# Optimization experiments

Measured on AMD Instinct MI355X. Metric: run time of the kernel, lower is better.

## Reference

```python
import jax, jax.numpy as jnp
import numpy as np

EMBED_DIM = 1024
N_HEADS = 16


def setup_inputs() -> dict:
    key = jax.random.key(0)
    k1, k2, k3 = jax.random.split(key, 3)
    B, T, C = 4, 2048, EMBED_DIM
    x0 = jax.random.normal(k1, (B, T, C), dtype=jnp.float32)
    # Linear weights stored as (in, out) so y = x @ W, matching torch Linear math.
    w_attn = jax.random.normal(k2, (C, 3 * C), dtype=jnp.float32) * (1.0 / np.sqrt(C))
    w_proj = jax.random.normal(k3, (C, C), dtype=jnp.float32) * (1.0 / np.sqrt(C))
    return {"x0": x0, "w_attn": w_attn, "w_proj": w_proj}


def reference(x0, w_attn, w_proj):
    B, T, C = x0.shape
    H = N_HEADS
    D = C // H  # head dim
    qkv = x0 @ w_attn                      # [B, T, 3C]
    q, k, v = jnp.split(qkv, 3, axis=-1)
    # [B, T, C] -> [B, H, T, D]
    q = q.reshape(B, T, H, D).transpose(0, 2, 1, 3)
    k = k.reshape(B, T, H, D).transpose(0, 2, 1, 3)
    v = v.reshape(B, T, H, D).transpose(0, 2, 1, 3)
    scale = 1.0 / np.sqrt(D)
    attn = jnp.einsum('bhqd,bhkd->bhqk', q, k) * scale  # [B, H, T, T]
    causal = jnp.tril(jnp.ones((T, T), dtype=bool))
    attn = jnp.where(causal[None, None, :, :], attn, -jnp.inf)
    attn = jax.nn.softmax(attn, axis=-1)
    y = jnp.einsum('bhqk,bhkd->bhqd', attn, v)           # [B, H, T, D]
    y = y.transpose(0, 2, 1, 3).reshape(B, T, C)
    return y @ w_proj
```

## Files before the change

### kernel.cpp

```cpp
#include <hip/hip_runtime.h>

#define TSEQ 2048
#define NB 4
#define NH 16
#define HD 64
#define CEMB 1024
#define MROWS (NB*TSEQ)

typedef _Float16 half8 __attribute__((ext_vector_type(8)));
typedef _Float16 half4_t __attribute__((ext_vector_type(4)));
typedef float floatx4 __attribute__((ext_vector_type(4)));

__device__ __forceinline__ floatx4 mfma16x32(half8 a, half8 b, floatx4 c) {
    return __builtin_amdgcn_mfma_f32_16x16x32_f16(a, b, c, 0, 0, 0);
}

__device__ __forceinline__ void async16(const _Float16* g, _Float16* l) {
    __builtin_amdgcn_global_load_lds((const __attribute__((address_space(1))) void*)g,
                                     (__attribute__((address_space(3))) void*)l, 16, 0, 0);
}

__global__ __launch_bounds__(256) void cvt_fp32_fp16(const float* __restrict__ in,
                                                     _Float16* __restrict__ out) {
    size_t i = ((size_t)blockIdx.x * 256 + threadIdx.x) * 8;
    float4 a = *(const float4*)(in + i);
    float4 b = *(const float4*)(in + i + 4);
    half8 h;
    h[0] = (_Float16)a.x; h[1] = (_Float16)a.y; h[2] = (_Float16)a.z; h[3] = (_Float16)a.w;
    h[4] = (_Float16)b.x; h[5] = (_Float16)b.y; h[6] = (_Float16)b.z; h[7] = (_Float16)b.w;
    *(half8*)(out + i) = h;
}

__global__ __launch_bounds__(256) void transpose_cvt(const float* __restrict__ in,
                                                     _Float16* __restrict__ out,
                                                     int R, int Ccols) {
    __shared__ float tile[32][33];
    int bx = blockIdx.x;
    int by = blockIdx.y;
    int tx = threadIdx.x, ty = threadIdx.y;
    int x = bx * 32 + tx;
#pragma unroll
    for (int i = 0; i < 32; i += 8) {
        int y = by * 32 + ty + i;
        tile[ty + i][tx] = in[(size_t)y * Ccols + x];
    }
    __syncthreads();
#pragma unroll
    for (int i = 0; i < 32; i += 8) {
        int oc = bx * 32 + ty + i;
        int orow = by * 32 + tx;
        out[(size_t)oc * R + orow] = (_Float16)tile[tx][ty + i];
    }
}

template<int MODE, int BM>
__global__ __launch_bounds__(BM * 2, 4) void gemm_nt(const _Float16* __restrict__ A,
                                                     const _Float16* __restrict__ Bt,
                                                     float* __restrict__ Cf,
                                                     _Float16* __restrict__ Ch,
                                                     _Float16* __restrict__ VTh,
                                                     int N, int K) {
    __shared__ __align__(16) _Float16 As[2][BM * 32];
    __shared__ __align__(16) _Float16 Bs[2][4096];

    const int tid = threadIdx.x;
    const int wv = tid >> 6, lane = tid & 63;
    const int wm = (BM == 256) ? (wv & 3) : (wv >> 1);
    const int wn = (BM == 256) ? (wv >> 2) : (wv & 1);
    const int l16 = lane & 15, lq = lane >> 4;

    const int pid = blockIdx.x + gridDim.x * blockIdx.y;
    const int nn = gridDim.y;
    const int pig = 8 * nn;
    const int gid = pid / pig;
    const int rem = pid - gid * pig;
    const int bm = gid * 8 + (rem & 7);
    const int bn = rem >> 3;

    const int srow = lane >> 2;
    const int scol = ((lane & 3) ^ ((lane >> 3) & 3)) * 8;
    const _Float16* Abase = A + (size_t)(bm * BM) * K;
    const _Float16* Bbase = Bt + (size_t)(bn * 128) * K;

    const floatx4 zero = {0.f, 0.f, 0.f, 0.f};
    floatx4 acc[4][4];
#pragma unroll
    for (int i = 0; i < 4; i++)
#pragma unroll
        for (int j = 0; j < 4; j++) acc[i][j] = zero;

    auto stage = [&](int bf, int k0) {
#pragma unroll
        for (int cc = 0; cc < 2; cc++) {
            const int c = wv * 2 + cc;
            const size_t gofs = (size_t)(c * 16 + srow) * K + k0 + scol;
            async16(Abase + gofs, &As[bf][c * 512]);
        }
        if (BM == 256) {
            const int c = wv;
            const size_t gofs = (size_t)(c * 16 + srow) * K + k0 + scol;
            async16(Bbase + gofs, &Bs[bf][c * 512]);
        } else {
#pragma unroll
            for (int cc = 0; cc < 2; cc++) {
                const int c = wv * 2 + cc;
                const size_t gofs = (size_t)(c * 16 + srow) * K + k0 + scol;
                async16(Bbase + gofs, &Bs[bf][c * 512]);
            }
        }
    };

    stage(0, 0);
    int buf = 0;
    const int sw = (lq ^ ((l16 >> 1) & 3)) * 8;
    for (int k0 = 0; k0 < K; k0 += 32) {
        __syncthreads();
        if (k0 + 32 < K) stage(buf ^ 1, k0 + 32);
        half8 af[4], bf[4];
#pragma unroll
        for (int i = 0; i < 4; i++) {
            af[i] = *(const half8*)&As[buf][(wm * 64 + i * 16 + l16) * 32 + sw];
            bf[i] = *(const half8*)&Bs[buf][(wn * 64 + i * 16 + l16) * 32 + sw];
        }
#pragma unroll
        for (int i = 0; i < 4; i++)
#pragma unroll
            for (int j = 0; j < 4; j++)
                acc[i][j] = mfma16x32(af[i], bf[j], acc[i][j]);
        buf ^= 1;
    }

    if (MODE == 1) {
#pragma unroll
        for (int i = 0; i < 4; i++) {
            int row = bm * BM + wm * 64 + i * 16 + lq * 4;
#pragma unroll
            for (int j = 0; j < 4; j++) {
                int col = bn * 128 + wn * 64 + j * 16 + l16;
#pragma unroll
                for (int r = 0; r < 4; r++)
                    Cf[(size_t)(row + r) * N + col] = acc[i][j][r];
            }
        }
    } else {
        const int which = bn >> 3;
        if (which < 2) {
#pragma unroll
            for (int j = 0; j < 4; j++) {
                int n = bn * 128 + wn * 64 + j * 16 + l16;
                int c = n & 1023, h = c >> 6, d = c & 63;
                _Float16* dst = Ch + (size_t)which * ((size_t)MROWS * CEMB)
                                   + (size_t)h * (TSEQ * HD) + d;
#pragma unroll
                for (int i = 0; i < 4; i++) {
                    int row = bm * BM + wm * 64 + i * 16 + lq * 4;
#pragma unroll
                    for (int r = 0; r < 4; r++) {
                        int m = row + r;
                        int b = m >> 11, t = m & 2047;
                        dst[(size_t)b * (NH * TSEQ * HD) + (size_t)t * HD] = (_Float16)acc[i][j][r];
                    }
                }
            }
        } else {
#pragma unroll
            for (int j = 0; j < 4; j++) {
                int n = bn * 128 + wn * 64 + j * 16 + l16;
                int c = n & 1023, h = c >> 6, d = c & 63;
#pragma unroll
                for (int i = 0; i < 4; i++) {
                    int m0 = bm * BM + wm * 64 + i * 16 + lq * 4;
                    int b = m0 >> 11, t = m0 & 2047;
                    half4_t pk;
#pragma unroll
                    for (int r = 0; r < 4; r++) pk[r] = (_Float16)acc[i][j][r];
                    *(half4_t*)&VTh[(((size_t)(b * NH + h)) * HD + d) * TSEQ + t] = pk;
                }
            }
        }
    }
}

__global__ __launch_bounds__(512, 4) void attn_fwd(const _Float16* __restrict__ Qg,
                                                   const _Float16* __restrict__ Kg,
                                                   const _Float16* __restrict__ VTg,
                                                   _Float16* __restrict__ Y) {
    __shared__ __align__(16) _Float16 Ks[2][4096];
    __shared__ __align__(16) _Float16 Vt[2][4096];

    const int tid = threadIdx.x;
    const int w = tid >> 6, lane = tid & 63;
    const int l16 = lane & 15, quad = lane >> 4;
    const int bh = blockIdx.y;
    const int x = blockIdx.x;
    const int b = bh >> 4, h = bh & 15;
    const int qt = (b < 2) ? x : (7 - x);

    const _Float16* Qb = Qg + (size_t)bh * TSEQ * HD;
    const _Float16* Kb = Kg + (size_t)bh * TSEQ * HD;
    const _Float16* Vb = VTg + (size_t)bh * HD * TSEQ;

    const _Float16 ksc = (_Float16)(0.125f * 1.44269504089f);
    const floatx4 zero = {0.f, 0.f, 0.f, 0.f};

    half8 qf[2][2];
#pragma unroll
    for (int g = 0; g < 2; g++) {
        const _Float16* qrow = Qb + (size_t)(qt * 256 + g * 128 + w * 16 + l16) * HD;
        qf[g][0] = *(const half8*)(qrow + quad * 8);
        qf[g][1] = *(const half8*)(qrow + 32 + quad * 8);
#pragma unroll
        for (int e = 0; e < 8; e++) { qf[g][0][e] *= ksc; qf[g][1][e] *= ksc; }
    }

    floatx4 o[2][4];
#pragma unroll
    for (int g = 0; g < 2; g++)
#pragma unroll
        for (int dt = 0; dt < 4; dt++) o[g][dt] = zero;
    float lsum[2] = {0.f, 0.f};

    const int srow8 = lane >> 3;
    const int scol8 = ((lane & 7) ^ (lane >> 3)) * 8;

    auto stage = [&](int bf, int kt2) {
        const int row = w * 8 + srow8;
        async16(Kb + (size_t)(kt2 * 64 + row) * HD + scol8, &Ks[bf][w * 512]);
        async16(Vb + (size_t)row * TSEQ + kt2 * 64 + scol8, &Vt[bf][w * 512]);
    };

    const int kmax = 4 * qt + 3;
    stage(0, 0);
    int buf = 0;
    for (int kt = 0; kt <= kmax; ++kt) {
        __syncthreads();
        if (kt < kmax) stage(buf ^ 1, kt + 1);

        half8 kf0[4], kf1[4];
#pragma unroll
        for (int nj = 0; nj < 4; nj++) {
            const int rb = (nj * 16 + l16) * 64;
            kf0[nj] = *(const half8*)&Ks[buf][rb + ((quad ^ (l16 & 7)) * 8)];
            kf1[nj] = *(const half8*)&Ks[buf][rb + (((quad ^ 4) ^ (l16 & 7)) * 8)];
        }

        const bool doA = (kt <= 4 * qt + 1);
        half8 pf[2][2];
#pragma unroll
        for (int g = 0; g < 2; g++) {
            if (g == 0 && !doA) continue;
            floatx4 st[4];
#pragma unroll
            for (int nj = 0; nj < 4; nj++) {
                floatx4 t = mfma16x32(kf0[nj], qf[g][0], zero);
                st[nj] = mfma16x32(kf1[nj], qf[g][1], t);
            }
            if (kt * 64 + 63 > qt * 256 + g * 128 + w * 16) {
                const int klim = qt * 256 + g * 128 + w * 16 + l16 - kt * 64;
#pragma unroll
                for (int nj = 0; nj < 4; nj++)
#pragma unroll
                    for (int r = 0; r < 4; r++) {
                        int key = nj * 16 + quad * 4 + r;
                        if (key > klim) st[nj][r] = -1e30f;
                    }
            }
#pragma unroll
            for (int nj = 0; nj < 4; nj++)
#pragma unroll
                for (int r = 0; r < 4; r++) {
                    float p = __builtin_amdgcn_exp2f(st[nj][r]);
                    lsum[g] += p;
                    pf[g][nj >> 1][(nj & 1) * 4 + r] = (_Float16)p;
                }
        }

#pragma unroll
        for (int u = 0; u < 2; u++) {
#pragma unroll
            for (int dt = 0; dt < 4; dt++) {
                const int rb = (dt * 16 + l16) * 64;
                const int g0 = u * 4 + (quad >> 1);
                const int sub = (quad & 1) * 4;
                half4_t lo = *(const half4_t*)&Vt[buf][rb + ((g0 ^ (l16 & 7)) * 8 + sub)];
                half4_t hi = *(const half4_t*)&Vt[buf][rb + (((g0 + 2) ^ (l16 & 7)) * 8 + sub)];
                half8 vf;
                vf[0] = lo[0]; vf[1] = lo[1]; vf[2] = lo[2]; vf[3] = lo[3];
                vf[4] = hi[0]; vf[5] = hi[1]; vf[6] = hi[2]; vf[7] = hi[3];
                if (doA) o[0][dt] = mfma16x32(pf[0][u], vf, o[0][dt]);
                o[1][dt] = mfma16x32(pf[1][u], vf, o[1][dt]);
            }
        }
        buf ^= 1;
    }

#pragma unroll
    for (int g = 0; g < 2; g++) {
        float lt = lsum[g];
        lt += __shfl_xor(lt, 16);
        lt += __shfl_xor(lt, 32);
        float linv[4];
#pragma unroll
        for (int r = 0; r < 4; r++) linv[r] = 1.0f / __shfl(lt, quad * 4 + r);
#pragma unroll
        for (int dt = 0; dt < 4; dt++)
#pragma unroll
            for (int r = 0; r < 4; r++) {
                int q = qt * 256 + g * 128 + w * 16 + quad * 4 + r;
                int d = dt * 16 + l16;
                Y[((size_t)(b * TSEQ + q)) * CEMB + h * HD + d] = (_Float16)(o[g][dt][r] * linv[r]);
            }
    }
}

extern "C" void kernel_launch(void* const* d_in, const int* in_sizes, int n_in,
                              void* d_out, int out_size, void* d_ws, size_t ws_size,
                              hipStream_t stream) {
    const float* x0     = (const float*)d_in[0];
    const float* w_attn = (const float*)d_in[1];
    const float* w_proj = (const float*)d_in[2];
    float* out = (float*)d_out;

    _Float16* xh  = (_Float16*)d_ws;
    _Float16* wqt = xh  + (size_t)MROWS * CEMB;
    _Float16* wpt = wqt + (size_t)3 * CEMB * CEMB;
    _Float16* qh  = wpt + (size_t)CEMB * CEMB;
    _Float16* kh  = qh  + (size_t)MROWS * CEMB;
    _Float16* vt  = kh  + (size_t)MROWS * CEMB;
    _Float16* yh  = vt  + (size_t)MROWS * CEMB;

    cvt_fp32_fp16<<<(MROWS * CEMB) / (256 * 8), 256, 0, stream>>>(x0, xh);
    transpose_cvt<<<dim3(3 * CEMB / 32, CEMB / 32), dim3(32, 8), 0, stream>>>(w_attn, wqt, CEMB, 3 * CEMB);
    transpose_cvt<<<dim3(CEMB / 32, CEMB / 32), dim3(32, 8), 0, stream>>>(w_proj, wpt, CEMB, CEMB);

    gemm_nt<0, 256><<<dim3(MROWS / 256, 3 * CEMB / 128), 512, 0, stream>>>(xh, wqt, nullptr, qh, vt, 3 * CEMB, CEMB);
    attn_fwd<<<dim3(TSEQ / 256, NB * NH), 512, 0, stream>>>(qh, kh, vt, yh);
    gemm_nt<1, 128><<<dim3(MROWS / 128, CEMB / 128), 256, 0, stream>>>(yh, wpt, out, nullptr, nullptr, CEMB, CEMB);
}
```

Measured before the change: 252.5 us.

## Rewrite GEMM as 4-stage async pipeline with 128x256 tiles

Replaces the double-buffered GEMM with a four-slot LDS ring that prefetches three k-steps ahead, using explicit vmcnt waits, raw barriers, scheduling barriers and raised priority around the MFMA block. Both the QKV and output projections now use 128x256 output tiles with 512 threads, each warp holding a 64x64 sub-tile. The aim is to hide global-load latency behind matrix math and cut the number of block-wide syncs. In exchange it uses more LDS per block, which lowers occupancy, and the output projection gets fewer, larger blocks.

```diff
diff --git a/kernel.cpp b/kernel.cpp
--- a/kernel.cpp
+++ b/kernel.cpp
@@ -53,21 +53,20 @@
     }
 }
 
-template<int MODE, int BM>
-__global__ __launch_bounds__(BM * 2, 4) void gemm_nt(const _Float16* __restrict__ A,
-                                                     const _Float16* __restrict__ Bt,
-                                                     float* __restrict__ Cf,
-                                                     _Float16* __restrict__ Ch,
-                                                     _Float16* __restrict__ VTh,
-                                                     int N, int K) {
-    __shared__ __align__(16) _Float16 As[2][BM * 32];
-    __shared__ __align__(16) _Float16 Bs[2][4096];
+template<int MODE>
+__global__ __launch_bounds__(512, 2) void gemm_nt8(const _Float16* __restrict__ A,
+                                                   const _Float16* __restrict__ Bt,
+                                                   float* __restrict__ Cf,
+                                                   _Float16* __restrict__ Ch,
+                                                   _Float16* __restrict__ VTh,
+                                                   int N, int K) {
+    __shared__ __align__(16) _Float16 As[4][128 * 32];
+    __shared__ __align__(16) _Float16 Bs[4][256 * 32];
 
     const int tid = threadIdx.x;
     const int wv = tid >> 6, lane = tid & 63;
-    const int wm = (BM == 256) ? (wv & 3) : (wv >> 1);
-    const int wn = (BM == 256) ? (wv >> 2) : (wv & 1);
-    const int l16 = lane & 15, lq = lane >> 4;
+    const int wm = wv >> 2, wn = wv & 3;
+    const int l16 = lane & 15, quad = lane >> 4;
 
     const int pid = blockIdx.x + gridDim.x * blockIdx.y;
     const int nn = gridDim.y;
@@ -77,10 +76,17 @@
     const int bm = gid * 8 + (rem & 7);
     const int bn = rem >> 3;
 
-    const int srow = lane >> 2;
-    const int scol = ((lane & 3) ^ ((lane >> 3) & 3)) * 8;
-    const _Float16* Abase = A + (size_t)(bm * BM) * K;
-    const _Float16* Bbase = Bt + (size_t)(bn * 128) * K;
+    const int rA = tid >> 2;
+    const int kA = ((tid & 3) ^ ((rA >> 1) & 3)) * 8;
+    const _Float16* Ag  = A  + (size_t)(bm * 128 + rA) * K + kA;
+    const _Float16* Bg0 = Bt + (size_t)(bn * 256 + rA) * K + kA;
+    const _Float16* Bg1 = Bg0 + (size_t)128 * K;
+
+    auto stage = [&](int slot, int ss) {
+        async16(Ag  + ss * 32, &As[slot][wv * 512]);
+        async16(Bg0 + ss * 32, &Bs[slot][wv * 512]);
+        async16(Bg1 + ss * 32, &Bs[slot][4096 + wv * 512]);
+    };
 
     const floatx4 zero = {0.f, 0.f, 0.f, 0.f};
     floatx4 acc[4][4];
@@ -89,71 +95,62 @@
 #pragma unroll
         for (int j = 0; j < 4; j++) acc[i][j] = zero;
 
-    auto stage = [&](int bf, int k0) {
-#pragma unroll
-        for (int cc = 0; cc < 2; cc++) {
-            const int c = wv * 2 + cc;
-            const size_t gofs = (size_t)(c * 16 + srow) * K + k0 + scol;
-            async16(Abase + gofs, &As[bf][c * 512]);
-        }
-        if (BM == 256) {
-            const int c = wv;
-            const size_t gofs = (size_t)(c * 16 + srow) * K + k0 + scol;
-            async16(Bbase + gofs, &Bs[bf][c * 512]);
-        } else {
-#pragma unroll
-            for (int cc = 0; cc < 2; cc++) {
-                const int c = wv * 2 + cc;
-                const size_t gofs = (size_t)(c * 16 + srow) * K + k0 + scol;
-                async16(Bbase + gofs, &Bs[bf][c * 512]);
-            }
-        }
-    };
-
-    stage(0, 0);
-    int buf = 0;
-    const int sw = (lq ^ ((l16 >> 1) & 3)) * 8;
-    for (int k0 = 0; k0 < K; k0 += 32) {
-        __syncthreads();
-        if (k0 + 32 < K) stage(buf ^ 1, k0 + 32);
-        half8 af[4], bf[4];
+    const int sw2 = (quad ^ ((l16 >> 1) & 3)) * 8;
+    const int offA = (wm * 64 + l16) * 32 + sw2;
+    const int offB = (wn * 64 + l16) * 32 + sw2;
+
+    stage(0, 0); stage(1, 1); stage(2, 2);
+    asm volatile("s_waitcnt vmcnt(6)\n\ts_barrier" ::: "memory");
+
+    const int NS = K >> 5;
+    for (int it = 0; it < NS / 4; ++it) {
+#pragma unroll
+        for (int p = 0; p < 4; ++p) {
+            const int s = it * 4 + p;
+            half8 af[4], bf[4];
+#pragma unroll
+            for (int i = 0; i < 4; i++) af[i] = *(const half8*)&As[p][offA + i * 512];
+#pragma unroll
+            for (int j = 0; j < 4; j++) bf[j] = *(const half8*)&Bs[p][offB + j * 512];
+            if (s + 3 < NS) stage((p + 3) & 3, s + 3);
+            asm volatile("s_barrier" ::: "memory");
+            __builtin_amdgcn_sched_barrier(0);
+            __builtin_amdgcn_s_setprio(1);
+#pragma unroll
+            for (int i = 0; i < 4; i++)
+#pragma unroll
+                for (int j = 0; j < 4; j++)
+                    acc[i][j] = mfma16x32(af[i], bf[j], acc[i][j]);
+            __builtin_amdgcn_s_setprio(0);
+            __builtin_amdgcn_sched_barrier(0);
+            asm volatile("s_waitcnt vmcnt(6)\n\ts_barrier" ::: "memory");
+        }
+    }
+
+    if (MODE == 1) {
 #pragma unroll
         for (int i = 0; i < 4; i++) {
-            af[i] = *(const half8*)&As[buf][(wm * 64 + i * 16 + l16) * 32 + sw];
-            bf[i] = *(const half8*)&Bs[buf][(wn * 64 + i * 16 + l16) * 32 + sw];
-        }
-#pragma unroll
-        for (int i = 0; i < 4; i++)
-#pragma unroll
-            for (int j = 0; j < 4; j++)
-                acc[i][j] = mfma16x32(af[i], bf[j], acc[i][j]);
-        buf ^= 1;
-    }
-
-    if (MODE == 1) {
-#pragma unroll
-        for (int i = 0; i < 4; i++) {
-            int row = bm * BM + wm * 64 + i * 16 + lq * 4;
+            int row = bm * 128 + wm * 64 + i * 16 + quad * 4;
 #pragma unroll
             for (int j = 0; j < 4; j++) {
-                int col = bn * 128 + wn * 64 + j * 16 + l16;
+                int col = bn * 256 + wn * 64 + j * 16 + l16;
 #pragma unroll
                 for (int r = 0; r < 4; r++)
                     Cf[(size_t)(row + r) * N + col] = acc[i][j][r];
             }
         }
     } else {
-        const int which = bn >> 3;
+        const int which = bn >> 2;
         if (which < 2) {
 #pragma unroll
             for (int j = 0; j < 4; j++) {
-                int n = bn * 128 + wn * 64 + j * 16 + l16;
+                int n = bn * 256 + wn * 64 + j * 16 + l16;
                 int c = n & 1023, h = c >> 6, d = c & 63;
                 _Float16* dst = Ch + (size_t)which * ((size_t)MROWS * CEMB)
                                    + (size_t)h * (TSEQ * HD) + d;
 #pragma unroll
                 for (int i = 0; i < 4; i++) {
-                    int row = bm * BM + wm * 64 + i * 16 + lq * 4;
+                    int row = bm * 128 + wm * 64 + i * 16 + quad * 4;
 #pragma unroll
                     for (int r = 0; r < 4; r++) {
                         int m = row + r;
@@ -165,11 +162,11 @@
         } else {
 #pragma unroll
             for (int j = 0; j < 4; j++) {
-                int n = bn * 128 + wn * 64 + j * 16 + l16;
+                int n = bn * 256 + wn * 64 + j * 16 + l16;
                 int c = n & 1023, h = c >> 6, d = c & 63;
 #pragma unroll
                 for (int i = 0; i < 4; i++) {
-                    int m0 = bm * BM + wm * 64 + i * 16 + lq * 4;
+                    int m0 = bm * 128 + wm * 64 + i * 16 + quad * 4;
                     int b = m0 >> 11, t = m0 & 2047;
                     half4_t pk;
 #pragma unroll
@@ -333,7 +330,7 @@
     transpose_cvt<<<dim3(3 * CEMB / 32, CEMB / 32), dim3(32, 8), 0, stream>>>(w_attn, wqt, CEMB, 3 * CEMB);
     transpose_cvt<<<dim3(CEMB / 32, CEMB / 32), dim3(32, 8), 0, stream>>>(w_proj, wpt, CEMB, CEMB);
 
-    gemm_nt<0, 256><<<dim3(MROWS / 256, 3 * CEMB / 128), 512, 0, stream>>>(xh, wqt, nullptr, qh, vt, 3 * CEMB, CEMB);
+    gemm_nt8<0><<<dim3(MROWS / 128, 3 * CEMB / 256), 512, 0, stream>>>(xh, wqt, nullptr, qh, vt, 3 * CEMB, CEMB);
     attn_fwd<<<dim3(TSEQ / 256, NB * NH), 512, 0, stream>>>(qh, kh, vt, yh);
-    gemm_nt<1, 128><<<dim3(MROWS / 128, CEMB / 128), 256, 0, stream>>>(yh, wpt, out, nullptr, nullptr, CEMB, CEMB);
-}
+    gemm_nt8<1><<<dim3(MROWS / 128, CEMB / 256), 512, 0, stream>>>(yh, wpt, out, nullptr, nullptr, CEMB, CEMB);
+}
```

New measurement: 242.6 us. 1.04x faster.
